# Kernel tuning notes

Measured on AMD Instinct MI355X. Metric: run time of the kernel, lower is better.

The kernel has to match this reference:

```python
import jax, jax.numpy as jnp
from jax import lax
import numpy as np

WIN = 11
PAD = WIN // 2
SIGMA = 1.5
GAMMA = 50.0


def _gauss_1d():
    x = jnp.arange(WIN, dtype=jnp.float32) - PAD
    g = jnp.exp(-(x * x) / (2.0 * SIGMA * SIGMA))
    return g / jnp.sum(g)


def _dwconv_gauss(x):
    # depthwise separable 11x11 gaussian blur, zero ('SAME') padding, NCHW
    C = x.shape[1]
    g = _gauss_1d()
    kh = jnp.tile(g.reshape(1, 1, WIN, 1), (C, 1, 1, 1))
    kw = jnp.tile(g.reshape(1, 1, 1, WIN), (C, 1, 1, 1))
    dn = ('NCHW', 'OIHW', 'NCHW')
    x = lax.conv_general_dilated(x, kh, (1, 1), [(PAD, PAD), (0, 0)],
                                 dimension_numbers=dn, feature_group_count=C)
    x = lax.conv_general_dilated(x, kw, (1, 1), [(0, 0), (PAD, PAD)],
                                 dimension_numbers=dn, feature_group_count=C)
    return x


def ssim(img1, img2):
    C1, C2 = 0.01 ** 2, 0.03 ** 2
    mu1 = _dwconv_gauss(img1)
    mu2 = _dwconv_gauss(img2)
    mu1_sq, mu2_sq, mu12 = mu1 * mu1, mu2 * mu2, mu1 * mu2
    sigma1_sq = _dwconv_gauss(img1 * img1) - mu1_sq
    sigma2_sq = _dwconv_gauss(img2 * img2) - mu2_sq
    sigma12 = _dwconv_gauss(img1 * img2) - mu12
    ssim_map = ((2 * mu12 + C1) * (2 * sigma12 + C2)) / (
        (mu1_sq + mu2_sq + C1) * (sigma1_sq + sigma2_sq + C2))
    return jnp.mean(ssim_map)


def warp(img, disp, x_dist, y_dist):
    # bilinear sample img at (x + x_dist*disp, y + y_dist*disp), border clamp
    B, C, H, W = img.shape
    d = disp[:, 0]  # [B,H,W]
    xs = jnp.arange(W, dtype=img.dtype)[None, None, :]
    ys = jnp.arange(H, dtype=img.dtype)[None, :, None]
    xn = jnp.clip(xs + x_dist * d, 0.0, W - 1.0)
    yn = jnp.clip(ys + y_dist * d, 0.0, H - 1.0)
    x0 = jnp.floor(xn)
    y0 = jnp.floor(yn)
    wx = xn - x0
    wy = yn - y0
    x0i = x0.astype(jnp.int32)
    y0i = y0.astype(jnp.int32)
    x1i = jnp.minimum(x0i + 1, W - 1)
    y1i = jnp.minimum(y0i + 1, H - 1)
    imh = jnp.transpose(img, (0, 2, 3, 1))  # [B,H,W,C]
    b = jnp.arange(B)[:, None, None]
    v00 = imh[b, y0i, x0i]
    v01 = imh[b, y0i, x1i]
    v10 = imh[b, y1i, x0i]
    v11 = imh[b, y1i, x1i]
    wx = wx[..., None]
    wy = wy[..., None]
    out = (v00 * (1 - wx) * (1 - wy) + v01 * wx * (1 - wy)
           + v10 * (1 - wx) * wy + v11 * wx * wy)
    return jnp.transpose(out, (0, 3, 1, 2))


def smooth_loss(disp, img, gamma):
    ddx = jnp.abs(disp[:, :, :, :-1] - disp[:, :, :, 1:])
    ddy = jnp.abs(disp[:, :, :-1, :] - disp[:, :, 1:, :])
    idx = jnp.mean(jnp.abs(img[:, :, :, :-1] - img[:, :, :, 1:]), axis=1, keepdims=True)
    idy = jnp.mean(jnp.abs(img[:, :, :-1, :] - img[:, :, 1:, :]), axis=1, keepdims=True)
    return jnp.mean(ddx * jnp.exp(-gamma * idx)) + jnp.mean(ddy * jnp.exp(-gamma * idy))


def l1(a, b):
    return jnp.mean(jnp.abs(a - b))


def setup_inputs() -> dict:
    key = jax.random.key(0)
    ks = jax.random.split(key, 8)
    B, H, W = 8, 512, 1024
    MAXD = 64.0
    return {
        'disp_l': jax.random.uniform(ks[0], (B, 1, H, W), jnp.float32) * MAXD,
        'disp_r': jax.random.uniform(ks[1], (B, 1, H, W), jnp.float32) * MAXD,
        'disp_ld2': jax.random.uniform(ks[2], (B, 1, H // 2, W // 2), jnp.float32) * (MAXD / 2),
        'disp_rd2': jax.random.uniform(ks[3], (B, 1, H // 2, W // 2), jnp.float32) * (MAXD / 2),
        'img_l': jax.random.uniform(ks[4], (B, 3, H, W), jnp.float32),
        'img_r': jax.random.uniform(ks[5], (B, 3, H, W), jnp.float32),
        'img_ld2': jax.random.uniform(ks[6], (B, 3, H // 2, W // 2), jnp.float32),
        'img_rd2': jax.random.uniform(ks[7], (B, 3, H // 2, W // 2), jnp.float32),
    }


def reference(disp_l, disp_r, disp_ld2, disp_rd2, img_l, img_r, img_ld2, img_rd2):
    img_ld2_warp = warp(img_rd2, disp_ld2, x_dist=-1.0, y_dist=0.0)
    img_rd2_warp = warp(img_ld2, disp_rd2, x_dist=1.0, y_dist=0.0)
    pm_d2 = l1(img_ld2_warp, img_ld2) + l1(img_rd2_warp, img_rd2)
    smooth_d2 = smooth_loss(disp_ld2, img_ld2, GAMMA) + smooth_loss(disp_rd2, img_rd2, GAMMA)

    img_l_warp = warp(img_r, disp_l, x_dist=-1.0, y_dist=0.0)
    img_r_warp = warp(img_l, disp_r, x_dist=1.0, y_dist=0.0)
    pm = l1(img_l_warp, img_l) + l1(img_r_warp, img_r)
    smooth = smooth_loss(disp_l, img_l, GAMMA) + smooth_loss(disp_r, img_r, GAMMA)
    ssim_loss = 1.0 - (ssim(img_l_warp, img_l) + ssim(img_r_warp, img_r)) / 2.0

    full_loss = pm_d2 + 0.1 * smooth_d2 + pm + ssim_loss + 0.1 * smooth
    monitor_loss = 5.0 * pm + ssim_loss
    return (full_loss, monitor_loss)
```

## Files before the change

### kernel.cpp

```cpp
#include <hip/hip_runtime.h>

#define B_ 8
#define C_ 3
#define H_ 512
#define W_ 1024
#define H2_ 256
#define W2_ 512
#define GAMMA_ 50.0f
#define NSUB 4

typedef __attribute__((ext_vector_type(2))) float v2f;


template <int NV>
__device__ __forceinline__ void reduce_acc(float (&v)[NV], double* acc, const int (&qidx)[NV]) {
    __shared__ float sred[NV][4];
    const int lane = threadIdx.x & 63;
    const int wave = threadIdx.x >> 6;
#pragma unroll
    for (int o = 32; o > 0; o >>= 1)
#pragma unroll
        for (int q = 0; q < NV; q++) v[q] += __shfl_down(v[q], o, 64);
    if (lane == 0)
#pragma unroll
        for (int q = 0; q < NV; q++) sred[q][wave] = v[q];
    __syncthreads();
    if (threadIdx.x == 0) {
        const int sub = blockIdx.x & (NSUB - 1);
#pragma unroll
        for (int q = 0; q < NV; q++) {
            float s = sred[q][0] + sred[q][1] + sred[q][2] + sred[q][3];
            atomicAdd(&acc[qidx[q] * NSUB + sub], (double)s);
        }
    }
}

__global__ void init_acc(double* acc) {
    if (threadIdx.x < 7 * NSUB) acc[threadIdx.x] = 0.0;
}

#define G0 0.0010283804f
#define G1 0.0075987582f
#define G2 0.0360007882f
#define G3 0.1093606949f
#define G4 0.2130055428f
#define G5 0.2660117248f

#define TH 16
#define TW 64
#define HALO_H (TH + 10)
#define HALO_W (TW + 10)
#define HALO_N (HALO_H * HALO_W)
#define VW 75

#define NHALF (B_ * H2_ * (W2_ / 4))
#define NSMOOTH (B_ * H_ * (W_ / 4))
#define NTOT (NHALF + NSMOOTH)
#define NSMALLBLK 1024
#define NSSIMBLK 8192

__device__ __forceinline__ int swz(int ridx) {
    return ridx ^ (((ridx >> 3) & 1) << 1) ^ ((ridx >> 4) & 1);
}

__global__ __launch_bounds__(256) void fused_kernel(
    const float* __restrict__ disp_l, const float* __restrict__ disp_r,
    const float* __restrict__ dL2, const float* __restrict__ dR2,
    const float* __restrict__ img_l, const float* __restrict__ img_r,
    const float* __restrict__ iL2, const float* __restrict__ iR2, double* acc) {
    __shared__ float2 sAB[HALO_N];
    __shared__ float4 vF[TH * VW];

    const int bid = blockIdx.x;
    const int grp = bid / 9;
    const int rem = bid - grp * 9;

    if (rem == 8) {
        float pm = 0.f, sx2 = 0.f, sy2 = 0.f, sxf = 0.f, syf = 0.f;
        for (int i = grp * blockDim.x + threadIdx.x; i < NTOT;
             i += NSMALLBLK * blockDim.x) {
            if (i < NHALF) {
                const int W4 = W2_ >> 2;
                const int HW = H2_ * W2_;
                const int xq = i % W4;
                const int x4 = xq << 2;
                const int yz = i / W4;
                const int y = yz % H2_;
                const int b = yz / H2_;
                const int p0 = (b * H2_ + y) * W2_ + x4;
                const int ib = ((b * C_) * H2_ + y) * W2_ + x4;
                const bool lastx = (x4 + 4 == W2_);
                const bool lasty = (y == H2_ - 1);

                float dl[5], dr[5];
                *(float4*)dl = *(const float4*)(dL2 + p0);
                *(float4*)dr = *(const float4*)(dR2 + p0);
                dl[4] = lastx ? 0.f : dL2[p0 + 4];
                dr[4] = lastx ? 0.f : dR2[p0 + 4];

                int xl0[4], xl1[4], xr0[4], xr1[4];
                float wxl[4], wxr[4];
#pragma unroll
                for (int t = 0; t < 4; t++) {
                    float xn = fminf(fmaxf((float)(x4 + t) - dl[t], 0.f), (float)(W2_ - 1));
                    float xf = floorf(xn);
                    wxl[t] = xn - xf;
                    xl0[t] = (int)xf;
                    xl1[t] = xl0[t] + (xl0[t] < W2_ - 1 ? 1 : 0);
                    float xm = fminf(fmaxf((float)(x4 + t) + dr[t], 0.f), (float)(W2_ - 1));
                    float xg = floorf(xm);
                    wxr[t] = xm - xg;
                    xr0[t] = (int)xg;
                    xr1[t] = xr0[t] + (xr0[t] < W2_ - 1 ? 1 : 0);
                }

                float axL[4] = {0, 0, 0, 0}, axR[4] = {0, 0, 0, 0};
                float ayL[4] = {0, 0, 0, 0}, ayR[4] = {0, 0, 0, 0};
#pragma unroll
                for (int ch = 0; ch < C_; ch++) {
                    const float* pL = iL2 + ib + ch * HW;
                    const float* pR = iR2 + ib + ch * HW;
                    float vL[5], vR[5];
                    *(float4*)vL = *(const float4*)pL;
                    *(float4*)vR = *(const float4*)pR;
                    vL[4] = lastx ? 0.f : pL[4];
                    vR[4] = lastx ? 0.f : pR[4];
#pragma unroll
                    for (int t = 0; t < 4; t++) {
                        axL[t] += fabsf(vL[t] - vL[t + 1]);
                        axR[t] += fabsf(vR[t] - vR[t + 1]);
                    }
                    if (!lasty) {
                        float wLr[4], wRr[4];
                        *(float4*)wLr = *(const float4*)(pL + W2_);
                        *(float4*)wRr = *(const float4*)(pR + W2_);
#pragma unroll
                        for (int t = 0; t < 4; t++) {
                            ayL[t] += fabsf(vL[t] - wLr[t]);
                            ayR[t] += fabsf(vR[t] - wRr[t]);
                        }
                    }
                    const float* gLrow = iR2 + ib - x4 + ch * HW;
                    const float* gRrow = iL2 + ib - x4 + ch * HW;
#pragma unroll
                    for (int t = 0; t < 4; t++) {
                        float wv = gLrow[xl0[t]] * (1.f - wxl[t]) + gLrow[xl1[t]] * wxl[t];
                        pm += fabsf(wv - vL[t]);
                        float wv2 = gRrow[xr0[t]] * (1.f - wxr[t]) + gRrow[xr1[t]] * wxr[t];
                        pm += fabsf(wv2 - vR[t]);
                    }
                }
                const int nx = lastx ? 3 : 4;
#pragma unroll
                for (int t = 0; t < 4; t++) {
                    if (t < nx) {
                        sx2 += fabsf(dl[t] - dl[t + 1]) * __expf(-GAMMA_ * (axL[t] * (1.f / 3.f)));
                        sx2 += fabsf(dr[t] - dr[t + 1]) * __expf(-GAMMA_ * (axR[t] * (1.f / 3.f)));
                    }
                }
                if (!lasty) {
                    float el[4], er[4];
                    *(float4*)el = *(const float4*)(dL2 + p0 + W2_);
                    *(float4*)er = *(const float4*)(dR2 + p0 + W2_);
#pragma unroll
                    for (int t = 0; t < 4; t++) {
                        sy2 += fabsf(dl[t] - el[t]) * __expf(-GAMMA_ * (ayL[t] * (1.f / 3.f)));
                        sy2 += fabsf(dr[t] - er[t]) * __expf(-GAMMA_ * (ayR[t] * (1.f / 3.f)));
                    }
                }
            } else {
                const int s = i - NHALF;
                const int W4 = W_ >> 2;
                const int HW = H_ * W_;
                const int xq = s % W4;
                const int x4 = xq << 2;
                const int yz = s / W4;
                const int y = yz % H_;
                const int b = yz / H_;
                const int p0 = (b * H_ + y) * W_ + x4;
                const int ib = ((b * C_) * H_ + y) * W_ + x4;
                const bool lastx = (x4 + 4 == W_);
                const bool lasty = (y == H_ - 1);

                float axL[4] = {0, 0, 0, 0}, axR[4] = {0, 0, 0, 0};
                float ayL[4] = {0, 0, 0, 0}, ayR[4] = {0, 0, 0, 0};
#pragma unroll
                for (int ch = 0; ch < C_; ch++) {
                    const float* pL = img_l + ib + ch * HW;
                    const float* pR = img_r + ib + ch * HW;
                    float vL[5], vR[5];
                    *(float4*)vL = *(const float4*)pL;
                    *(float4*)vR = *(const float4*)pR;
                    vL[4] = lastx ? 0.f : pL[4];
                    vR[4] = lastx ? 0.f : pR[4];
#pragma unroll
                    for (int t = 0; t < 4; t++) {
                        axL[t] += fabsf(vL[t] - vL[t + 1]);
                        axR[t] += fabsf(vR[t] - vR[t + 1]);
                    }
                    if (!lasty) {
                        float wLr[4], wRr[4];
                        *(float4*)wLr = *(const float4*)(pL + W_);
                        *(float4*)wRr = *(const float4*)(pR + W_);
#pragma unroll
                        for (int t = 0; t < 4; t++) {
                            ayL[t] += fabsf(vL[t] - wLr[t]);
                            ayR[t] += fabsf(vR[t] - wRr[t]);
                        }
                    }
                }
                float dl[5], dr[5];
                *(float4*)dl = *(const float4*)(disp_l + p0);
                *(float4*)dr = *(const float4*)(disp_r + p0);
                dl[4] = lastx ? 0.f : disp_l[p0 + 4];
                dr[4] = lastx ? 0.f : disp_r[p0 + 4];
                const int nx = lastx ? 3 : 4;
#pragma unroll
                for (int t = 0; t < 4; t++) {
                    if (t < nx) {
                        sxf += fabsf(dl[t] - dl[t + 1]) * __expf(-GAMMA_ * (axL[t] * (1.f / 3.f)));
                        sxf += fabsf(dr[t] - dr[t + 1]) * __expf(-GAMMA_ * (axR[t] * (1.f / 3.f)));
                    }
                }
                if (!lasty) {
                    float el[4], er[4];
                    *(float4*)el = *(const float4*)(disp_l + p0 + W_);
                    *(float4*)er = *(const float4*)(disp_r + p0 + W_);
#pragma unroll
                    for (int t = 0; t < 4; t++) {
                        syf += fabsf(dl[t] - el[t]) * __expf(-GAMMA_ * (ayL[t] * (1.f / 3.f)));
                        syf += fabsf(dr[t] - er[t]) * __expf(-GAMMA_ * (ayR[t] * (1.f / 3.f)));
                    }
                }
            }
        }
        float vals[5] = {pm, sx2, sy2, sxf, syf};
        const int qidx[5] = {0, 1, 2, 4, 5};
        reduce_acc<5>(vals, acc, qidx);
        return;
    }

    const int xcd = (grp + rem) & 7;
    const int t8 = grp >> 3;
    const int idx = rem * 128 + t8;
    const int z = idx >> 6;
    const int r6 = idx & 63;
    const int by = (xcd << 2) | (r6 >> 4);
    const int bx = r6 & 15;

    const int b = z >> 1;
    const int pair = z & 1;
    const float* samp = (pair == 0) ? img_r : img_l;
    const float* targ = (pair == 0) ? img_l : img_r;
    const float* disp = (pair == 0) ? disp_l : disp_r;
    const float sign = (pair == 0) ? -1.f : 1.f;

    const int x0t = bx * TW;
    const int y0t = by * TH;

    const float gg[11] = {G0, G1, G2, G3, G4, G5, G4, G3, G2, G1, G0};
    v2f w01[14], w23[14];
#pragma unroll
    for (int k = 0; k < 14; ++k) {
        w01[k].x = (k <= 10) ? gg[k] : 0.f;
        w01[k].y = (k >= 1 && k <= 11) ? gg[k - 1] : 0.f;
        w23[k].x = (k >= 2 && k <= 12) ? gg[k - 2] : 0.f;
        w23[k].y = (k >= 3) ? gg[k - 3] : 0.f;
    }

    int riy[8], gxa[8], gxb[8];
    float wxs[8];
    {
        const int bHW = b * (H_ * W_);
#pragma unroll
        for (int it = 0; it < 8; ++it) {
            const int idq = threadIdx.x + 256 * it;
            riy[it] = -1;
            if (idq < HALO_N) {
                const int i = idq / HALO_W;
                const int j = idq - i * HALO_W;
                const int iy = y0t + i - 5;
                const int ix = x0t + j - 5;
                if (iy >= 0 && iy < H_ && ix >= 0 && ix < W_) {
                    const int rr = iy * W_ + ix;
                    riy[it] = rr;
                    const float d = disp[bHW + rr];
                    float xn = fminf(fmaxf((float)ix + sign * d, 0.f), (float)(W_ - 1));
                    float xf = floorf(xn);
                    wxs[it] = xn - xf;
                    const int xi = (int)xf;
                    gxa[it] = iy * W_ + xi;
                    gxb[it] = gxa[it] + (xi < W_ - 1 ? 1 : 0);
                }
            }
        }
    }

    float pa0[8], pa1[8], pbv[8];
    auto prefetch = [&](int c) {
        const int cb = (b * C_ + c) * (H_ * W_);
#pragma unroll
        for (int it = 0; it < 8; ++it) {
            const int idq = threadIdx.x + 256 * it;
            if (idq < HALO_N && riy[it] >= 0) {
                pbv[it] = targ[cb + riy[it]];
                pa0[it] = samp[cb + gxa[it]];
                pa1[it] = samp[cb + gxb[it]];
            }
        }
    };

    float ssim_loc = 0.f, pm_loc = 0.f;

    const int hr = threadIdx.x >> 4;
    const int hc0 = (threadIdx.x & 15) << 2;

    prefetch(0);

#pragma unroll 1
    for (int c = 0; c < C_; ++c) {
#pragma unroll
        for (int it = 0; it < 8; ++it) {
            const int idq = threadIdx.x + 256 * it;
            if (idq < HALO_N) {
                float av = 0.f, bv = 0.f;
                if (riy[it] >= 0) {
                    const float wx = wxs[it];
                    av = pa0[it] * (1.f - wx) + pa1[it] * wx;
                    bv = pbv[it];
                }
                sAB[idq] = make_float2(av, bv);
            }
        }
        __syncthreads();

        if (c + 1 < C_) prefetch(c + 1);

#pragma unroll
        for (int it = 0; it < 2; ++it) {
            const int t = threadIdx.x + 256 * it;
            if (t < 4 * HALO_W) {
                const int q = t / HALO_W;
                const int j = t - q * HALO_W;
                const int r0 = q * 4;
                const bool jc = (j >= 5 && j < 69);
                v2f amA = 0.f, bmA = 0.f, ssA = 0.f, abA = 0.f;
                v2f amB = 0.f, bmB = 0.f, ssB = 0.f, abB = 0.f;
#pragma unroll
                for (int k = 0; k < 14; ++k) {
                    const float2 p = sAB[(r0 + k) * HALO_W + j];
                    const float sq = fmaf(p.y, p.y, p.x * p.x);
                    const float ab = p.x * p.y;
                    const v2f wA = w01[k], wB = w23[k];
                    amA += wA * p.x;
                    bmA += wA * p.y;
                    ssA += wA * sq;
                    abA += wA * ab;
                    amB += wB * p.x;
                    bmB += wB * p.y;
                    ssB += wB * sq;
                    abB += wB * ab;
                    if (k >= 5 && k <= 8) {
                        if (jc) pm_loc += fabsf(p.x - p.y);
                    }
                }
                const int rb = r0 * VW + j;
                vF[swz(rb)] = make_float4(amA.x, bmA.x, ssA.x, abA.x);
                vF[swz(rb + VW)] = make_float4(amA.y, bmA.y, ssA.y, abA.y);
                vF[swz(rb + 2 * VW)] = make_float4(amB.x, bmB.x, ssB.x, abB.x);
                vF[swz(rb + 3 * VW)] = make_float4(amB.y, bmB.y, ssB.y, abB.y);
            }
        }
        __syncthreads();

        {
            const int rowb = hr * VW + hc0;
            v2f m1A = 0.f, m2A = 0.f, qsA = 0.f, q12A = 0.f;
            v2f m1B = 0.f, m2B = 0.f, qsB = 0.f, q12B = 0.f;
#pragma unroll
            for (int k = 0; k < 14; ++k) {
                const float4 f = vF[swz(rowb + k)];
                const v2f wA = w01[k], wB = w23[k];
                m1A += wA * f.x;
                m2A += wA * f.y;
                qsA += wA * f.z;
                q12A += wA * f.w;
                m1B += wB * f.x;
                m2B += wB * f.y;
                qsB += wB * f.z;
                q12B += wB * f.w;
            }
            const float C1 = 1e-4f, C2 = 9e-4f;
            {
                const v2f mu1sq = m1A * m1A, mu2sq = m2A * m2A, mu12 = m1A * m2A;
                const v2f s12 = q12A - mu12, ss = qsA - mu1sq - mu2sq;
                const v2f num = (2.f * mu12 + C1) * (2.f * s12 + C2);
                const v2f den = (mu1sq + mu2sq + C1) * (ss + C2);
                const v2f r = num / den;
                ssim_loc += r.x + r.y;
            }
            {
                const v2f mu1sq = m1B * m1B, mu2sq = m2B * m2B, mu12 = m1B * m2B;
                const v2f s12 = q12B - mu12, ss = qsB - mu1sq - mu2sq;
                const v2f num = (2.f * mu12 + C1) * (2.f * s12 + C2);
                const v2f den = (mu1sq + mu2sq + C1) * (ss + C2);
                const v2f r = num / den;
                ssim_loc += r.x + r.y;
            }
        }
    }

    float vals[2] = {ssim_loc, pm_loc};
    const int qidx[2] = {6, 3};
    reduce_acc<2>(vals, acc, qidx);
}

__global__ void finalize_kernel(const double* __restrict__ acc, float* __restrict__ out) {
    if (threadIdx.x == 0 && blockIdx.x == 0) {
        double q[7];
        for (int i = 0; i < 7; i++) {
            q[i] = 0.0;
            for (int s = 0; s < NSUB; s++) q[i] += acc[i * NSUB + s];
        }
        const double N2 = (double)B_ * C_ * H2_ * W2_;
        const double Nx2 = (double)B_ * H2_ * (W2_ - 1);
        const double Ny2 = (double)B_ * (H2_ - 1) * W2_;
        const double N1 = (double)B_ * C_ * H_ * W_;
        const double Nx1 = (double)B_ * H_ * (W_ - 1);
        const double Ny1 = (double)B_ * (H_ - 1) * W_;
        double pm_d2 = q[0] / N2;
        double smooth_d2 = q[1] / Nx2 + q[2] / Ny2;
        double pm = q[3] / N1;
        double smooth = q[4] / Nx1 + q[5] / Ny1;
        double ssim_loss = 1.0 - q[6] / (2.0 * N1);
        double full = pm_d2 + 0.1 * smooth_d2 + pm + ssim_loss + 0.1 * smooth;
        double mon = 5.0 * pm + ssim_loss;
        out[0] = (float)full;
        out[1] = (float)mon;
    }
}

extern "C" void kernel_launch(void* const* d_in, const int* in_sizes, int n_in,
                              void* d_out, int out_size, void* d_ws, size_t ws_size,
                              hipStream_t stream) {
    const float* disp_l = (const float*)d_in[0];
    const float* disp_r = (const float*)d_in[1];
    const float* disp_ld2 = (const float*)d_in[2];
    const float* disp_rd2 = (const float*)d_in[3];
    const float* img_l = (const float*)d_in[4];
    const float* img_r = (const float*)d_in[5];
    const float* img_ld2 = (const float*)d_in[6];
    const float* img_rd2 = (const float*)d_in[7];
    double* acc = (double*)d_ws;
    float* out = (float*)d_out;

    hipLaunchKernelGGL(init_acc, dim3(1), dim3(64), 0, stream, acc);

    hipLaunchKernelGGL(fused_kernel, dim3(NSSIMBLK + NSMALLBLK), dim3(256), 0, stream,
                       disp_l, disp_r, disp_ld2, disp_rd2,
                       img_l, img_r, img_ld2, img_rd2, acc);

    hipLaunchKernelGGL(finalize_kernel, dim3(1), dim3(1), 0, stream, acc, out);
}
```

Baseline: 193.3 us.

## Fold smoothness and half-res photometric work into SSIM blocks instead of separate blocks

Removes the dedicated grid-stride blocks that computed half-resolution photometric loss and smoothness terms, and instead has each SSIM tile block process one extra element per thread after its SSIM work. The block-to-tile mapping is simplified accordingly and the per-block reduction grows from two to seven values. This aims to eliminate the extra blocks, their strided loop and separate atomics, and to overlap memory-bound smoothness work with SSIM compute. It risks higher register pressure in the SSIM kernel and uneven tail work, since only the first blocks carry extra elements.

Result: slower. 346.6 us (+79.3%).

```diff
diff --git a/kernel.cpp b/kernel.cpp
--- a/kernel.cpp
+++ b/kernel.cpp
@@ -26,11 +26,10 @@
         for (int q = 0; q < NV; q++) sred[q][wave] = v[q];
     __syncthreads();
     if (threadIdx.x == 0) {
-        const int sub = blockIdx.x & (NSUB - 1);
 #pragma unroll
         for (int q = 0; q < NV; q++) {
             float s = sred[q][0] + sred[q][1] + sred[q][2] + sred[q][3];
-            atomicAdd(&acc[qidx[q] * NSUB + sub], (double)s);
+            atomicAdd(&acc[qidx[q] * NSUB + (blockIdx.x & (NSUB - 1))], (double)s);
         }
     }
 }
@@ -56,7 +55,6 @@
 #define NHALF (B_ * H2_ * (W2_ / 4))
 #define NSMOOTH (B_ * H_ * (W_ / 4))
 #define NTOT (NHALF + NSMOOTH)
-#define NSMALLBLK 1024
 #define NSSIMBLK 8192
 
 __device__ __forceinline__ int swz(int ridx) {
@@ -72,179 +70,11 @@
     __shared__ float4 vF[TH * VW];
 
     const int bid = blockIdx.x;
-    const int grp = bid / 9;
-    const int rem = bid - grp * 9;
-
-    if (rem == 8) {
-        float pm = 0.f, sx2 = 0.f, sy2 = 0.f, sxf = 0.f, syf = 0.f;
-        for (int i = grp * blockDim.x + threadIdx.x; i < NTOT;
-             i += NSMALLBLK * blockDim.x) {
-            if (i < NHALF) {
-                const int W4 = W2_ >> 2;
-                const int HW = H2_ * W2_;
-                const int xq = i % W4;
-                const int x4 = xq << 2;
-                const int yz = i / W4;
-                const int y = yz % H2_;
-                const int b = yz / H2_;
-                const int p0 = (b * H2_ + y) * W2_ + x4;
-                const int ib = ((b * C_) * H2_ + y) * W2_ + x4;
-                const bool lastx = (x4 + 4 == W2_);
-                const bool lasty = (y == H2_ - 1);
-
-                float dl[5], dr[5];
-                *(float4*)dl = *(const float4*)(dL2 + p0);
-                *(float4*)dr = *(const float4*)(dR2 + p0);
-                dl[4] = lastx ? 0.f : dL2[p0 + 4];
-                dr[4] = lastx ? 0.f : dR2[p0 + 4];
-
-                int xl0[4], xl1[4], xr0[4], xr1[4];
-                float wxl[4], wxr[4];
-#pragma unroll
-                for (int t = 0; t < 4; t++) {
-                    float xn = fminf(fmaxf((float)(x4 + t) - dl[t], 0.f), (float)(W2_ - 1));
-                    float xf = floorf(xn);
-                    wxl[t] = xn - xf;
-                    xl0[t] = (int)xf;
-                    xl1[t] = xl0[t] + (xl0[t] < W2_ - 1 ? 1 : 0);
-                    float xm = fminf(fmaxf((float)(x4 + t) + dr[t], 0.f), (float)(W2_ - 1));
-                    float xg = floorf(xm);
-                    wxr[t] = xm - xg;
-                    xr0[t] = (int)xg;
-                    xr1[t] = xr0[t] + (xr0[t] < W2_ - 1 ? 1 : 0);
-                }
-
-                float axL[4] = {0, 0, 0, 0}, axR[4] = {0, 0, 0, 0};
-                float ayL[4] = {0, 0, 0, 0}, ayR[4] = {0, 0, 0, 0};
-#pragma unroll
-                for (int ch = 0; ch < C_; ch++) {
-                    const float* pL = iL2 + ib + ch * HW;
-                    const float* pR = iR2 + ib + ch * HW;
-                    float vL[5], vR[5];
-                    *(float4*)vL = *(const float4*)pL;
-                    *(float4*)vR = *(const float4*)pR;
-                    vL[4] = lastx ? 0.f : pL[4];
-                    vR[4] = lastx ? 0.f : pR[4];
-#pragma unroll
-                    for (int t = 0; t < 4; t++) {
-                        axL[t] += fabsf(vL[t] - vL[t + 1]);
-                        axR[t] += fabsf(vR[t] - vR[t + 1]);
-                    }
-                    if (!lasty) {
-                        float wLr[4], wRr[4];
-                        *(float4*)wLr = *(const float4*)(pL + W2_);
-                        *(float4*)wRr = *(const float4*)(pR + W2_);
-#pragma unroll
-                        for (int t = 0; t < 4; t++) {
-                            ayL[t] += fabsf(vL[t] - wLr[t]);
-                            ayR[t] += fabsf(vR[t] - wRr[t]);
-                        }
-                    }
-                    const float* gLrow = iR2 + ib - x4 + ch * HW;
-                    const float* gRrow = iL2 + ib - x4 + ch * HW;
-#pragma unroll
-                    for (int t = 0; t < 4; t++) {
-                        float wv = gLrow[xl0[t]] * (1.f - wxl[t]) + gLrow[xl1[t]] * wxl[t];
-                        pm += fabsf(wv - vL[t]);
-                        float wv2 = gRrow[xr0[t]] * (1.f - wxr[t]) + gRrow[xr1[t]] * wxr[t];
-                        pm += fabsf(wv2 - vR[t]);
-                    }
-                }
-                const int nx = lastx ? 3 : 4;
-#pragma unroll
-                for (int t = 0; t < 4; t++) {
-                    if (t < nx) {
-                        sx2 += fabsf(dl[t] - dl[t + 1]) * __expf(-GAMMA_ * (axL[t] * (1.f / 3.f)));
-                        sx2 += fabsf(dr[t] - dr[t + 1]) * __expf(-GAMMA_ * (axR[t] * (1.f / 3.f)));
-                    }
-                }
-                if (!lasty) {
-                    float el[4], er[4];
-                    *(float4*)el = *(const float4*)(dL2 + p0 + W2_);
-                    *(float4*)er = *(const float4*)(dR2 + p0 + W2_);
-#pragma unroll
-                    for (int t = 0; t < 4; t++) {
-                        sy2 += fabsf(dl[t] - el[t]) * __expf(-GAMMA_ * (ayL[t] * (1.f / 3.f)));
-                        sy2 += fabsf(dr[t] - er[t]) * __expf(-GAMMA_ * (ayR[t] * (1.f / 3.f)));
-                    }
-                }
-            } else {
-                const int s = i - NHALF;
-                const int W4 = W_ >> 2;
-                const int HW = H_ * W_;
-                const int xq = s % W4;
-                const int x4 = xq << 2;
-                const int yz = s / W4;
-                const int y = yz % H_;
-                const int b = yz / H_;
-                const int p0 = (b * H_ + y) * W_ + x4;
-                const int ib = ((b * C_) * H_ + y) * W_ + x4;
-                const bool lastx = (x4 + 4 == W_);
-                const bool lasty = (y == H_ - 1);
-
-                float axL[4] = {0, 0, 0, 0}, axR[4] = {0, 0, 0, 0};
-                float ayL[4] = {0, 0, 0, 0}, ayR[4] = {0, 0, 0, 0};
-#pragma unroll
-                for (int ch = 0; ch < C_; ch++) {
-                    const float* pL = img_l + ib + ch * HW;
-                    const float* pR = img_r + ib + ch * HW;
-                    float vL[5], vR[5];
-                    *(float4*)vL = *(const float4*)pL;
-                    *(float4*)vR = *(const float4*)pR;
-                    vL[4] = lastx ? 0.f : pL[4];
-                    vR[4] = lastx ? 0.f : pR[4];
-#pragma unroll
-                    for (int t = 0; t < 4; t++) {
-                        axL[t] += fabsf(vL[t] - vL[t + 1]);
-                        axR[t] += fabsf(vR[t] - vR[t + 1]);
-                    }
-                    if (!lasty) {
-                        float wLr[4], wRr[4];
-                        *(float4*)wLr = *(const float4*)(pL + W_);
-                        *(float4*)wRr = *(const float4*)(pR + W_);
-#pragma unroll
-                        for (int t = 0; t < 4; t++) {
-                            ayL[t] += fabsf(vL[t] - wLr[t]);
-                            ayR[t] += fabsf(vR[t] - wRr[t]);
-                        }
-                    }
-                }
-                float dl[5], dr[5];
-                *(float4*)dl = *(const float4*)(disp_l + p0);
-                *(float4*)dr = *(const float4*)(disp_r + p0);
-                dl[4] = lastx ? 0.f : disp_l[p0 + 4];
-                dr[4] = lastx ? 0.f : disp_r[p0 + 4];
-                const int nx = lastx ? 3 : 4;
-#pragma unroll
-                for (int t = 0; t < 4; t++) {
-                    if (t < nx) {
-                        sxf += fabsf(dl[t] - dl[t + 1]) * __expf(-GAMMA_ * (axL[t] * (1.f / 3.f)));
-                        sxf += fabsf(dr[t] - dr[t + 1]) * __expf(-GAMMA_ * (axR[t] * (1.f / 3.f)));
-                    }
-                }
-                if (!lasty) {
-                    float el[4], er[4];
-                    *(float4*)el = *(const float4*)(disp_l + p0 + W_);
-                    *(float4*)er = *(const float4*)(disp_r + p0 + W_);
-#pragma unroll
-                    for (int t = 0; t < 4; t++) {
-                        syf += fabsf(dl[t] - el[t]) * __expf(-GAMMA_ * (ayL[t] * (1.f / 3.f)));
-                        syf += fabsf(dr[t] - er[t]) * __expf(-GAMMA_ * (ayR[t] * (1.f / 3.f)));
-                    }
-                }
-            }
-        }
-        float vals[5] = {pm, sx2, sy2, sxf, syf};
-        const int qidx[5] = {0, 1, 2, 4, 5};
-        reduce_acc<5>(vals, acc, qidx);
-        return;
-    }
-
-    const int xcd = (grp + rem) & 7;
-    const int t8 = grp >> 3;
-    const int idx = rem * 128 + t8;
-    const int z = idx >> 6;
-    const int r6 = idx & 63;
+
+    const int xcd = bid & 7;
+    const int t8 = bid >> 3;
+    const int z = t8 >> 6;
+    const int r6 = t8 & 63;
     const int by = (xcd << 2) | (r6 >> 4);
     const int bx = r6 & 15;
 
@@ -410,9 +240,168 @@
         }
     }
 
-    float vals[2] = {ssim_loc, pm_loc};
-    const int qidx[2] = {6, 3};
-    reduce_acc<2>(vals, acc, qidx);
+    float pm2 = 0.f, sx2 = 0.f, sy2 = 0.f, sxf = 0.f, syf = 0.f;
+    {
+        const int i = bid * 256 + threadIdx.x;
+        if (i < NHALF) {
+            const int W4 = W2_ >> 2;
+            const int HW = H2_ * W2_;
+            const int xq = i % W4;
+            const int x4 = xq << 2;
+            const int yz = i / W4;
+            const int y = yz % H2_;
+            const int b2 = yz / H2_;
+            const int p0 = (b2 * H2_ + y) * W2_ + x4;
+            const int ib = ((b2 * C_) * H2_ + y) * W2_ + x4;
+            const bool lastx = (x4 + 4 == W2_);
+            const bool lasty = (y == H2_ - 1);
+
+            float dl[5], dr[5];
+            *(float4*)dl = *(const float4*)(dL2 + p0);
+            *(float4*)dr = *(const float4*)(dR2 + p0);
+            dl[4] = lastx ? 0.f : dL2[p0 + 4];
+            dr[4] = lastx ? 0.f : dR2[p0 + 4];
+
+            int xl0[4], xl1[4], xr0[4], xr1[4];
+            float wxl[4], wxr[4];
+#pragma unroll
+            for (int t = 0; t < 4; t++) {
+                float xn = fminf(fmaxf((float)(x4 + t) - dl[t], 0.f), (float)(W2_ - 1));
+                float xf = floorf(xn);
+                wxl[t] = xn - xf;
+                xl0[t] = (int)xf;
+                xl1[t] = xl0[t] + (xl0[t] < W2_ - 1 ? 1 : 0);
+                float xm = fminf(fmaxf((float)(x4 + t) + dr[t], 0.f), (float)(W2_ - 1));
+                float xg = floorf(xm);
+                wxr[t] = xm - xg;
+                xr0[t] = (int)xg;
+                xr1[t] = xr0[t] + (xr0[t] < W2_ - 1 ? 1 : 0);
+            }
+
+            float axL[4] = {0, 0, 0, 0}, axR[4] = {0, 0, 0, 0};
+            float ayL[4] = {0, 0, 0, 0}, ayR[4] = {0, 0, 0, 0};
+#pragma unroll
+            for (int ch = 0; ch < C_; ch++) {
+                const float* pL = iL2 + ib + ch * HW;
+                const float* pR = iR2 + ib + ch * HW;
+                float vL[5], vR[5];
+                *(float4*)vL = *(const float4*)pL;
+                *(float4*)vR = *(const float4*)pR;
+                vL[4] = lastx ? 0.f : pL[4];
+                vR[4] = lastx ? 0.f : pR[4];
+#pragma unroll
+                for (int t = 0; t < 4; t++) {
+                    axL[t] += fabsf(vL[t] - vL[t + 1]);
+                    axR[t] += fabsf(vR[t] - vR[t + 1]);
+                }
+                if (!lasty) {
+                    float wLr[4], wRr[4];
+                    *(float4*)wLr = *(const float4*)(pL + W2_);
+                    *(float4*)wRr = *(const float4*)(pR + W2_);
+#pragma unroll
+                    for (int t = 0; t < 4; t++) {
+                        ayL[t] += fabsf(vL[t] - wLr[t]);
+                        ayR[t] += fabsf(vR[t] - wRr[t]);
+                    }
+                }
+                const float* gLrow = iR2 + ib - x4 + ch * HW;
+                const float* gRrow = iL2 + ib - x4 + ch * HW;
+#pragma unroll
+                for (int t = 0; t < 4; t++) {
+                    float wv = gLrow[xl0[t]] * (1.f - wxl[t]) + gLrow[xl1[t]] * wxl[t];
+                    pm2 += fabsf(wv - vL[t]);
+                    float wv2 = gRrow[xr0[t]] * (1.f - wxr[t]) + gRrow[xr1[t]] * wxr[t];
+                    pm2 += fabsf(wv2 - vR[t]);
+                }
+            }
+            const int nx = lastx ? 3 : 4;
+#pragma unroll
+            for (int t = 0; t < 4; t++) {
+                if (t < nx) {
+                    sx2 += fabsf(dl[t] - dl[t + 1]) * __expf(-GAMMA_ * (axL[t] * (1.f / 3.f)));
+                    sx2 += fabsf(dr[t] - dr[t + 1]) * __expf(-GAMMA_ * (axR[t] * (1.f / 3.f)));
+                }
+            }
+            if (!lasty) {
+                float el[4], er[4];
+                *(float4*)el = *(const float4*)(dL2 + p0 + W2_);
+                *(float4*)er = *(const float4*)(dR2 + p0 + W2_);
+#pragma unroll
+                for (int t = 0; t < 4; t++) {
+                    sy2 += fabsf(dl[t] - el[t]) * __expf(-GAMMA_ * (ayL[t] * (1.f / 3.f)));
+                    sy2 += fabsf(dr[t] - er[t]) * __expf(-GAMMA_ * (ayR[t] * (1.f / 3.f)));
+                }
+            }
+        } else if (i < NTOT) {
+            const int s = i - NHALF;
+            const int W4 = W_ >> 2;
+            const int HW = H_ * W_;
+            const int xq = s % W4;
+            const int x4 = xq << 2;
+            const int yz = s / W4;
+            const int y = yz % H_;
+            const int b2 = yz / H_;
+            const int p0 = (b2 * H_ + y) * W_ + x4;
+            const int ib = ((b2 * C_) * H_ + y) * W_ + x4;
+            const bool lastx = (x4 + 4 == W_);
+            const bool lasty = (y == H_ - 1);
+
+            float axL[4] = {0, 0, 0, 0}, axR[4] = {0, 0, 0, 0};
+            float ayL[4] = {0, 0, 0, 0}, ayR[4] = {0, 0, 0, 0};
+#pragma unroll
+            for (int ch = 0; ch < C_; ch++) {
+                const float* pL = img_l + ib + ch * HW;
+                const float* pR = img_r + ib + ch * HW;
+                float vL[5], vR[5];
+                *(float4*)vL = *(const float4*)pL;
+                *(float4*)vR = *(const float4*)pR;
+                vL[4] = lastx ? 0.f : pL[4];
+                vR[4] = lastx ? 0.f : pR[4];
+#pragma unroll
+                for (int t = 0; t < 4; t++) {
+                    axL[t] += fabsf(vL[t] - vL[t + 1]);
+                    axR[t] += fabsf(vR[t] - vR[t + 1]);
+                }
+                if (!lasty) {
+                    float wLr[4], wRr[4];
+                    *(float4*)wLr = *(const float4*)(pL + W_);
+                    *(float4*)wRr = *(const float4*)(pR + W_);
+#pragma unroll
+                    for (int t = 0; t < 4; t++) {
+                        ayL[t] += fabsf(vL[t] - wLr[t]);
+                        ayR[t] += fabsf(vR[t] - wRr[t]);
+                    }
+                }
+            }
+            float dl[5], dr[5];
+            *(float4*)dl = *(const float4*)(disp_l + p0);
+            *(float4*)dr = *(const float4*)(disp_r + p0);
+            dl[4] = lastx ? 0.f : disp_l[p0 + 4];
+            dr[4] = lastx ? 0.f : disp_r[p0 + 4];
+            const int nx = lastx ? 3 : 4;
+#pragma unroll
+            for (int t = 0; t < 4; t++) {
+                if (t < nx) {
+                    sxf += fabsf(dl[t] - dl[t + 1]) * __expf(-GAMMA_ * (axL[t] * (1.f / 3.f)));
+                    sxf += fabsf(dr[t] - dr[t + 1]) * __expf(-GAMMA_ * (axR[t] * (1.f / 3.f)));
+                }
+            }
+            if (!lasty) {
+                float el[4], er[4];
+                *(float4*)el = *(const float4*)(disp_l + p0 + W_);
+                *(float4*)er = *(const float4*)(disp_r + p0 + W_);
+#pragma unroll
+                for (int t = 0; t < 4; t++) {
+                    syf += fabsf(dl[t] - el[t]) * __expf(-GAMMA_ * (ayL[t] * (1.f / 3.f)));
+                    syf += fabsf(dr[t] - er[t]) * __expf(-GAMMA_ * (ayR[t] * (1.f / 3.f)));
+                }
+            }
+        }
+    }
+
+    float vals[7] = {ssim_loc, pm_loc, pm2, sx2, sy2, sxf, syf};
+    const int qidx[7] = {6, 3, 0, 1, 2, 4, 5};
+    reduce_acc<7>(vals, acc, qidx);
 }
 
 __global__ void finalize_kernel(const double* __restrict__ acc, float* __restrict__ out) {
@@ -456,7 +445,7 @@
 
     hipLaunchKernelGGL(init_acc, dim3(1), dim3(64), 0, stream, acc);
 
-    hipLaunchKernelGGL(fused_kernel, dim3(NSSIMBLK + NSMALLBLK), dim3(256), 0, stream,
+    hipLaunchKernelGGL(fused_kernel, dim3(NSSIMBLK), dim3(256), 0, stream,
                        disp_l, disp_r, disp_ld2, disp_rd2,
                        img_l, img_r, img_ld2, img_rd2, acc);
 
```
